# Optimization experiments

Hardware: AMD Instinct MI355X
Metric: run time of the kernel (lower is better)

Reference implementation:

```python
import jax, jax.numpy as jnp
import numpy as np

N, F_IN, F_OUT = 10000, 256, 64
ALPHA = 0.2  # LeakyReLU negative slope
NEG_BIG = -9e15  # matches -9000000000000000.0 in the torch code


def setup_inputs() -> dict:
    key = jax.random.key(0)
    k1, k2, k3, k4 = jax.random.split(key, 4)
    h = jax.random.normal(k1, (N, F_IN), dtype=jnp.float32)
    adj = jax.random.randint(k2, (N, N), 0, 2, dtype=jnp.int32)
    # xavier-uniform-like scales for params
    W = jax.random.normal(k3, (F_IN, F_OUT), dtype=jnp.float32) * 0.08
    a = jax.random.normal(k4, (2 * F_OUT, 1), dtype=jnp.float32) * 0.1
    return {"h": h, "adj": adj, "W": W, "a": a}


def reference(h, adj, W, a):
    # Wh: [N, F_OUT]
    Wh = h @ W
    # Additive attention: e_ij = LeakyReLU(a1 . Wh_i + a2 . Wh_j)
    # This is mathematically identical to matmul([Wh_i || Wh_j], a) without
    # materializing the [N, N, 2*F_OUT] tensor.
    f1 = Wh @ a[:F_OUT]        # [N, 1] -> contribution of source node i
    f2 = Wh @ a[F_OUT:]        # [N, 1] -> contribution of target node j
    e = f1 + f2.T              # [N, N]
    e = jnp.where(e > 0, e, ALPHA * e)          # LeakyReLU
    e = jnp.where(adj > 0, e, NEG_BIG)          # adjacency masking
    attention = jax.nn.softmax(e, axis=1)       # masked softmax over neighbors
    # dropout is a no-op in eval mode (training=False)
    h_prime = attention @ Wh                    # [N, F_OUT]
    return jax.nn.elu(h_prime)                  # concat=True -> ELU
```

## Files before the change

kernel.cpp:

```cpp
#include <hip/hip_runtime.h>
#include <hip/hip_bf16.h>

#define N_NODES  10000
#define NPAD     10048
#define FIN      256
#define D        64
#define NTILE    157
#define ROWTILES 625
#define NSPLIT   8
#define ALPHA    0.2f

typedef __attribute__((ext_vector_type(8))) short bf16x8;
typedef __attribute__((ext_vector_type(4))) float f32x4;
typedef __attribute__((ext_vector_type(4))) int   i32x4;

__device__ __forceinline__ short bf16bits(float x) {
  union { __hip_bfloat16 b; short s; } u;
  u.b = __float2bfloat16(x);
  return u.s;
}
__device__ __forceinline__ unsigned flipf(float x) {
  unsigned u = __float_as_uint(x);
  return (u & 0x80000000u) ? ~u : (u | 0x80000000u);
}
__device__ __forceinline__ float unflipf(unsigned k) {
  return (k & 0x80000000u) ? __uint_as_float(k ^ 0x80000000u)
                           : __uint_as_float(~k);
}

__global__ __launch_bounds__(256) void k1_proj(
    const float* __restrict__ h, const float* __restrict__ W,
    const float* __restrict__ a,
    float* __restrict__ f1, float* __restrict__ f2,
    unsigned* __restrict__ f2maxW, short* __restrict__ whT) {
  int wid  = (blockIdx.x << 2) + (threadIdx.x >> 6);
  int lane = threadIdx.x & 63;
  if (wid >= NPAD) return;
  if (wid >= N_NODES) {
    whT[(size_t)lane * NPAD + wid] = 0;
    return;
  }
  const float* hrow = h + (size_t)wid * FIN;
  float acc = 0.f;
#pragma unroll 4
  for (int k = 0; k < FIN; k += 4) {
    float4 hv = *(const float4*)(hrow + k);
    acc += hv.x * W[(k + 0) * D + lane];
    acc += hv.y * W[(k + 1) * D + lane];
    acc += hv.z * W[(k + 2) * D + lane];
    acc += hv.w * W[(k + 3) * D + lane];
  }
  whT[(size_t)lane * NPAD + wid] = bf16bits(acc);
  float p1 = acc * a[lane];
  float p2 = acc * a[D + lane];
#pragma unroll
  for (int off = 32; off; off >>= 1) {
    p1 += __shfl_xor(p1, off);
    p2 += __shfl_xor(p2, off);
  }
  if (lane == 0) {
    f1[wid] = p1;
    f2[wid] = p2;
    atomicMax(f2maxW, flipf(p2));
  }
}

__global__ __launch_bounds__(256) void k2_attn(
    const int* __restrict__ adj, const float* __restrict__ f1,
    const float* __restrict__ f2, const unsigned* __restrict__ f2maxW,
    const short* __restrict__ whT,
    float* __restrict__ accW, float* __restrict__ sW) {
  int wg = (blockIdx.x << 2) + (threadIdx.x >> 6);
  if (wg >= ROWTILES * NSPLIT) return;
  int lane    = threadIdx.x & 63;
  int rowtile = wg % ROWTILES;
  int split   = wg / ROWTILES;
  int r = lane & 15;
  int g = lane >> 4;
  int row = rowtile * 16 + r;

  float f1r  = f1[row];
  float f2m  = unflipf(*f2maxW);
  float mraw = f1r + f2m;
  float Mhat = fmaxf(mraw, ALPHA * mraw);

  f32x4 acc[4];
#pragma unroll
  for (int cb = 0; cb < 4; ++cb) acc[cb] = (f32x4){0.f, 0.f, 0.f, 0.f};
  float s_part = 0.f;

  const int* adjrow = adj + (size_t)row * N_NODES;

  for (int t = split; t < NTILE; t += NSPLIT) {
    int j0 = t << 6;
    bf16x8 afrag[2];
#pragma unroll
    for (int ks = 0; ks < 2; ++ks) {
      int  jc  = j0 + ks * 32 + g * 8;
      bool inb = (jc < N_NODES);
      int  jcl = inb ? jc : (N_NODES - 8);
      i32x4 a0 = *(const i32x4*)(adjrow + jcl);
      i32x4 a1 = *(const i32x4*)(adjrow + jcl + 4);
      f32x4 F0 = *(const f32x4*)(f2 + jcl);
      f32x4 F1 = *(const f32x4*)(f2 + jcl + 4);
      float p[8];
#pragma unroll
      for (int e = 0; e < 4; ++e) {
        float e0 = f1r + F0[e];
        e0 = fmaxf(e0, ALPHA * e0);
        float pv0 = __expf(e0 - Mhat);
        p[e] = (inb && a0[e] != 0) ? pv0 : 0.f;
        float e1 = f1r + F1[e];
        e1 = fmaxf(e1, ALPHA * e1);
        float pv1 = __expf(e1 - Mhat);
        p[4 + e] = (inb && a1[e] != 0) ? pv1 : 0.f;
      }
#pragma unroll
      for (int e = 0; e < 8; ++e) s_part += p[e];
#pragma unroll
      for (int e = 0; e < 8; ++e) afrag[ks][e] = bf16bits(p[e]);
    }
#pragma unroll
    for (int ks = 0; ks < 2; ++ks) {
      const short* bbase = whT + (size_t)r * NPAD + j0 + ks * 32 + g * 8;
#pragma unroll
      for (int cb = 0; cb < 4; ++cb) {
        bf16x8 bfrag = *(const bf16x8*)(bbase + (size_t)cb * 16 * NPAD);
        acc[cb] = __builtin_amdgcn_mfma_f32_16x16x32_bf16(afrag[ks], bfrag,
                                                          acc[cb], 0, 0, 0);
      }
    }
  }

  s_part += __shfl_xor(s_part, 16);
  s_part += __shfl_xor(s_part, 32);

  int i0 = rowtile * 16;
#pragma unroll
  for (int cb = 0; cb < 4; ++cb)
#pragma unroll
    for (int q = 0; q < 4; ++q)
      atomicAdd(&accW[(size_t)(i0 + g * 4 + q) * D + cb * 16 + r], acc[cb][q]);
  if (lane < 16) atomicAdd(&sW[i0 + r], s_part);
}

__global__ __launch_bounds__(256) void k3_final(
    const float* __restrict__ accW, const float* __restrict__ sW,
    float* __restrict__ out) {
  int idx = blockIdx.x * 256 + threadIdx.x;
  if (idx >= N_NODES * D) return;
  float sv = fmaxf(sW[idx >> 6], 1e-30f);
  float v  = accW[idx] / sv;
  out[idx] = v > 0.f ? v : (__expf(v) - 1.f);
}

extern "C" void kernel_launch(void* const* d_in, const int* in_sizes, int n_in,
                              void* d_out, int out_size, void* d_ws, size_t ws_size,
                              hipStream_t stream) {
  const float* h   = (const float*)d_in[0];
  const int*   adj = (const int*)d_in[1];
  const float* W   = (const float*)d_in[2];
  const float* a   = (const float*)d_in[3];
  float* out = (float*)d_out;

  float* wsf = (float*)d_ws;
  float*    accW   = wsf;
  float*    sW     = wsf + 640000;
  unsigned* f2maxW = (unsigned*)(wsf + 650048);
  float*    f1W    = wsf + 650064;
  float*    f2W    = wsf + 660112;
  short*    whT    = (short*)(wsf + 670160);

  hipMemsetAsync(accW, 0, (size_t)650064 * sizeof(float), stream);

  hipLaunchKernelGGL(k1_proj, dim3(NPAD / 4), dim3(256), 0, stream,
                     h, W, a, f1W, f2W, f2maxW, whT);
  hipLaunchKernelGGL(k2_attn, dim3(ROWTILES * NSPLIT / 4), dim3(256), 0, stream,
                     adj, f1W, f2W, f2maxW, whT, accW, sW);
  hipLaunchKernelGGL(k3_final, dim3((N_NODES * D + 255) / 256), dim3(256), 0, stream,
                     accW, sW, out);
}
```

Measured before the change: 728.6 us.

## Stage attention tile through LDS and replace atomics with split partial buffers

The attention kernel now has each 256-thread block cooperatively compute a 16x256 tile of probabilities with fully coalesced adjacency row reads. The tile is written to swizzled LDS and consumed by four waves doing MFMA over disjoint column slices. The global float atomics and the memset are replaced by per-split partial accumulators, reduced in LDS within a block and across splits in the final kernel, and the f2 max moves from an atomicMax to a separate single-block reduction kernel. This adds block barriers, an extra launch and more workspace traffic in exchange for better adjacency coalescing and no atomics.

```diff
diff --git a/kernel.cpp b/kernel.cpp
--- a/kernel.cpp
+++ b/kernel.cpp
@@ -2,55 +2,47 @@
 #include <hip/hip_bf16.h>
 
 #define N_NODES  10000
-#define NPAD     10048
+#define NPAD     10240
 #define FIN      256
 #define D        64
-#define NTILE    157
+#define NT256    40
 #define ROWTILES 625
-#define NSPLIT   8
+#define NSPLIT   4
 #define ALPHA    0.2f
 
 typedef __attribute__((ext_vector_type(8))) short bf16x8;
 typedef __attribute__((ext_vector_type(4))) float f32x4;
 typedef __attribute__((ext_vector_type(4))) int   i32x4;
 
-__device__ __forceinline__ short bf16bits(float x) {
-  union { __hip_bfloat16 b; short s; } u;
+__device__ __forceinline__ unsigned bf16bits(float x) {
+  union { __hip_bfloat16 b; unsigned short s; } u;
   u.b = __float2bfloat16(x);
-  return u.s;
-}
-__device__ __forceinline__ unsigned flipf(float x) {
-  unsigned u = __float_as_uint(x);
-  return (u & 0x80000000u) ? ~u : (u | 0x80000000u);
-}
-__device__ __forceinline__ float unflipf(unsigned k) {
-  return (k & 0x80000000u) ? __uint_as_float(k ^ 0x80000000u)
-                           : __uint_as_float(~k);
+  return (unsigned)u.s;
 }
 
 __global__ __launch_bounds__(256) void k1_proj(
     const float* __restrict__ h, const float* __restrict__ W,
     const float* __restrict__ a,
     float* __restrict__ f1, float* __restrict__ f2,
-    unsigned* __restrict__ f2maxW, short* __restrict__ whT) {
+    short* __restrict__ whT) {
   int wid  = (blockIdx.x << 2) + (threadIdx.x >> 6);
   int lane = threadIdx.x & 63;
-  if (wid >= NPAD) return;
   if (wid >= N_NODES) {
-    whT[(size_t)lane * NPAD + wid] = 0;
+    if (wid < NPAD) whT[(size_t)lane * NPAD + wid] = 0;
     return;
   }
   const float* hrow = h + (size_t)wid * FIN;
-  float acc = 0.f;
+  float s0 = 0.f, s1 = 0.f, s2 = 0.f, s3 = 0.f;
 #pragma unroll 4
   for (int k = 0; k < FIN; k += 4) {
     float4 hv = *(const float4*)(hrow + k);
-    acc += hv.x * W[(k + 0) * D + lane];
-    acc += hv.y * W[(k + 1) * D + lane];
-    acc += hv.z * W[(k + 2) * D + lane];
-    acc += hv.w * W[(k + 3) * D + lane];
-  }
-  whT[(size_t)lane * NPAD + wid] = bf16bits(acc);
+    s0 += hv.x * W[(k + 0) * D + lane];
+    s1 += hv.y * W[(k + 1) * D + lane];
+    s2 += hv.z * W[(k + 2) * D + lane];
+    s3 += hv.w * W[(k + 3) * D + lane];
+  }
+  float acc = (s0 + s1) + (s2 + s3);
+  whT[(size_t)lane * NPAD + wid] = (short)bf16bits(acc);
   float p1 = acc * a[lane];
   float p2 = acc * a[D + lane];
 #pragma unroll
@@ -58,99 +50,134 @@
     p1 += __shfl_xor(p1, off);
     p2 += __shfl_xor(p2, off);
   }
-  if (lane == 0) {
-    f1[wid] = p1;
-    f2[wid] = p2;
-    atomicMax(f2maxW, flipf(p2));
-  }
+  if (lane == 0) { f1[wid] = p1; f2[wid] = p2; }
+}
+
+__global__ __launch_bounds__(256) void k1b_max(
+    const float* __restrict__ f2, float* __restrict__ f2maxF) {
+  float m = -3.4e38f;
+  for (int i = threadIdx.x; i < N_NODES; i += 256) m = fmaxf(m, f2[i]);
+#pragma unroll
+  for (int off = 32; off; off >>= 1) m = fmaxf(m, __shfl_xor(m, off));
+  __shared__ float wm[4];
+  if ((threadIdx.x & 63) == 0) wm[threadIdx.x >> 6] = m;
+  __syncthreads();
+  if (threadIdx.x == 0)
+    *f2maxF = fmaxf(fmaxf(wm[0], wm[1]), fmaxf(wm[2], wm[3]));
 }
 
 __global__ __launch_bounds__(256) void k2_attn(
     const int* __restrict__ adj, const float* __restrict__ f1,
-    const float* __restrict__ f2, const unsigned* __restrict__ f2maxW,
+    const float* __restrict__ f2, const float* __restrict__ f2maxF,
     const short* __restrict__ whT,
-    float* __restrict__ accW, float* __restrict__ sW) {
-  int wg = (blockIdx.x << 2) + (threadIdx.x >> 6);
-  if (wg >= ROWTILES * NSPLIT) return;
-  int lane    = threadIdx.x & 63;
-  int rowtile = wg % ROWTILES;
-  int split   = wg / ROWTILES;
-  int r = lane & 15;
-  int g = lane >> 4;
-  int row = rowtile * 16 + r;
-
-  float f1r  = f1[row];
-  float f2m  = unflipf(*f2maxW);
-  float mraw = f1r + f2m;
+    float* __restrict__ accP, float* __restrict__ sP) {
+  __shared__ float ldsF[4096];
+  char* ldsB = (char*)ldsF;
+  int tid = threadIdx.x;
+  int rowtile = blockIdx.x % ROWTILES;
+  int split   = blockIdx.x / ROWTILES;
+
+  int prow  = tid >> 4;
+  int cbase = (tid & 15) * 4;
+  int grow  = rowtile * 16 + prow;
+  float f1r  = f1[grow];
+  float mraw = f1r + *f2maxF;
   float Mhat = fmaxf(mraw, ALPHA * mraw);
+  const int* adjrow = adj + (size_t)grow * N_NODES;
+
+  int lane = tid & 63;
+  int w    = tid >> 6;
+  int r2   = lane & 15;
+  int g    = lane >> 4;
 
   f32x4 acc[4];
 #pragma unroll
   for (int cb = 0; cb < 4; ++cb) acc[cb] = (f32x4){0.f, 0.f, 0.f, 0.f};
-  float s_part = 0.f;
-
-  const int* adjrow = adj + (size_t)row * N_NODES;
-
-  for (int t = split; t < NTILE; t += NSPLIT) {
-    int j0 = t << 6;
-    bf16x8 afrag[2];
+  float sth = 0.f;
+
+  int pboff[4];
+#pragma unroll
+  for (int sub = 0; sub < 4; ++sub)
+    pboff[sub] = (prow * 512 + (cbase + sub * 64) * 2) ^ ((prow & 7) << 4);
+  int cboff[2];
+#pragma unroll
+  for (int ks = 0; ks < 2; ++ks)
+    cboff[ks] = (r2 * 512 + (w * 64 + ks * 32 + g * 8) * 2) ^ ((r2 & 7) << 4);
+  const short* bbase = whT + (size_t)r2 * NPAD + w * 64 + g * 8;
+
+  for (int tt = split; tt < NT256; tt += NSPLIT) {
+    int j0 = tt << 8;
+    i32x4 av[4]; f32x4 fv[4]; bool val[4];
+#pragma unroll
+    for (int sub = 0; sub < 4; ++sub) {
+      int j = j0 + cbase + sub * 64;
+      bool v = (j < N_NODES);
+      int jc = v ? j : (N_NODES - 4);
+      av[sub] = *(const i32x4*)(adjrow + jc);
+      fv[sub] = *(const f32x4*)(f2 + jc);
+      val[sub] = v;
+    }
+#pragma unroll
+    for (int sub = 0; sub < 4; ++sub) {
+      float p[4];
+#pragma unroll
+      for (int e = 0; e < 4; ++e) {
+        float ev = f1r + fv[sub][e];
+        ev = fmaxf(ev, ALPHA * ev);
+        float pv = __expf(ev - Mhat);
+        p[e] = (val[sub] && av[sub][e] != 0) ? pv : 0.f;
+        sth += p[e];
+      }
+      uint2 pk;
+      pk.x = bf16bits(p[0]) | (bf16bits(p[1]) << 16);
+      pk.y = bf16bits(p[2]) | (bf16bits(p[3]) << 16);
+      *(uint2*)(ldsB + pboff[sub]) = pk;
+    }
+    __syncthreads();
 #pragma unroll
     for (int ks = 0; ks < 2; ++ks) {
-      int  jc  = j0 + ks * 32 + g * 8;
-      bool inb = (jc < N_NODES);
-      int  jcl = inb ? jc : (N_NODES - 8);
-      i32x4 a0 = *(const i32x4*)(adjrow + jcl);
-      i32x4 a1 = *(const i32x4*)(adjrow + jcl + 4);
-      f32x4 F0 = *(const f32x4*)(f2 + jcl);
-      f32x4 F1 = *(const f32x4*)(f2 + jcl + 4);
-      float p[8];
-#pragma unroll
-      for (int e = 0; e < 4; ++e) {
-        float e0 = f1r + F0[e];
-        e0 = fmaxf(e0, ALPHA * e0);
-        float pv0 = __expf(e0 - Mhat);
-        p[e] = (inb && a0[e] != 0) ? pv0 : 0.f;
-        float e1 = f1r + F1[e];
-        e1 = fmaxf(e1, ALPHA * e1);
-        float pv1 = __expf(e1 - Mhat);
-        p[4 + e] = (inb && a1[e] != 0) ? pv1 : 0.f;
-      }
-#pragma unroll
-      for (int e = 0; e < 8; ++e) s_part += p[e];
-#pragma unroll
-      for (int e = 0; e < 8; ++e) afrag[ks][e] = bf16bits(p[e]);
-    }
-#pragma unroll
-    for (int ks = 0; ks < 2; ++ks) {
-      const short* bbase = whT + (size_t)r * NPAD + j0 + ks * 32 + g * 8;
+      bf16x8 af = *(const bf16x8*)(ldsB + cboff[ks]);
+      const short* bp = bbase + j0 + ks * 32;
 #pragma unroll
       for (int cb = 0; cb < 4; ++cb) {
-        bf16x8 bfrag = *(const bf16x8*)(bbase + (size_t)cb * 16 * NPAD);
-        acc[cb] = __builtin_amdgcn_mfma_f32_16x16x32_bf16(afrag[ks], bfrag,
-                                                          acc[cb], 0, 0, 0);
+        bf16x8 bf = *(const bf16x8*)(bp + (size_t)cb * 16 * NPAD);
+        acc[cb] = __builtin_amdgcn_mfma_f32_16x16x32_bf16(af, bf, acc[cb], 0, 0, 0);
       }
     }
-  }
-
-  s_part += __shfl_xor(s_part, 16);
-  s_part += __shfl_xor(s_part, 32);
-
-  int i0 = rowtile * 16;
+    __syncthreads();
+  }
+
+  sth += __shfl_xor(sth, 1);
+  sth += __shfl_xor(sth, 2);
+  sth += __shfl_xor(sth, 4);
+  sth += __shfl_xor(sth, 8);
+  if ((tid & 15) == 0) sP[split * N_NODES + grow] = sth;
+
+  float* accS = ldsF;
 #pragma unroll
   for (int cb = 0; cb < 4; ++cb)
 #pragma unroll
     for (int q = 0; q < 4; ++q)
-      atomicAdd(&accW[(size_t)(i0 + g * 4 + q) * D + cb * 16 + r], acc[cb][q]);
-  if (lane < 16) atomicAdd(&sW[i0 + r], s_part);
+      accS[(w * 16 + g * 4 + q) * 64 + cb * 16 + r2] = acc[cb][q];
+  __syncthreads();
+  int base = split * (N_NODES * D) + rowtile * 1024;
+#pragma unroll
+  for (int k = 0; k < 4; ++k) {
+    int o = tid + k * 256;
+    accP[base + o] = accS[o] + accS[1024 + o] + accS[2048 + o] + accS[3072 + o];
+  }
 }
 
 __global__ __launch_bounds__(256) void k3_final(
-    const float* __restrict__ accW, const float* __restrict__ sW,
+    const float* __restrict__ accP, const float* __restrict__ sP,
     float* __restrict__ out) {
   int idx = blockIdx.x * 256 + threadIdx.x;
   if (idx >= N_NODES * D) return;
-  float sv = fmaxf(sW[idx >> 6], 1e-30f);
-  float v  = accW[idx] / sv;
+  int row = idx >> 6;
+  float sv = (sP[row] + sP[N_NODES + row]) +
+             (sP[2 * N_NODES + row] + sP[3 * N_NODES + row]);
+  float v = ((accP[idx] + accP[640000 + idx]) +
+             (accP[1280000 + idx] + accP[1920000 + idx])) / sv;
   out[idx] = v > 0.f ? v : (__expf(v) - 1.f);
 }
 
@@ -164,19 +191,18 @@
   float* out = (float*)d_out;
 
   float* wsf = (float*)d_ws;
-  float*    accW   = wsf;
-  float*    sW     = wsf + 640000;
-  unsigned* f2maxW = (unsigned*)(wsf + 650048);
-  float*    f1W    = wsf + 650064;
-  float*    f2W    = wsf + 660112;
-  short*    whT    = (short*)(wsf + 670160);
-
-  hipMemsetAsync(accW, 0, (size_t)650064 * sizeof(float), stream);
+  float* accP   = wsf;
+  float* sP     = wsf + 2560000;
+  float* f2maxF = wsf + 2600000;
+  float* f1W    = wsf + 2600016;
+  float* f2W    = wsf + 2610032;
+  short* whT    = (short*)(wsf + 2620048);
 
   hipLaunchKernelGGL(k1_proj, dim3(NPAD / 4), dim3(256), 0, stream,
-                     h, W, a, f1W, f2W, f2maxW, whT);
-  hipLaunchKernelGGL(k2_attn, dim3(ROWTILES * NSPLIT / 4), dim3(256), 0, stream,
-                     adj, f1W, f2W, f2maxW, whT, accW, sW);
+                     h, W, a, f1W, f2W, whT);
+  hipLaunchKernelGGL(k1b_max, dim3(1), dim3(256), 0, stream, f2W, f2maxF);
+  hipLaunchKernelGGL(k2_attn, dim3(ROWTILES * NSPLIT), dim3(256), 0, stream,
+                     adj, f1W, f2W, f2maxF, whT, accP, sP);
   hipLaunchKernelGGL(k3_final, dim3((N_NODES * D + 255) / 256), dim3(256), 0, stream,
-                     accW, sW, out);
-}
+                     accP, sP, out);
+}
```

New measurement: 638.4 us. 12.4% less time.
